# Kernel optimization log

Hardware: AMD Instinct MI355X
Metric: run time of the kernel (lower is better)

The kernel has to match this reference:

```python
import jax, jax.numpy as jnp
import numpy as np

EPS = 1e-9
CAPACITY_FACTOR = 1.25
MIN_EXPERT_CAPACITY = 4
SECOND_THRESHOLD = 0.2
LOSS_COEF = 0.01

B, N, D, E, H = 4, 2048, 1024, 16, 4096


def setup_inputs() -> dict:
    key = jax.random.key(0)
    k_x, k_g, k_w1, k_w2, k_n = jax.random.split(key, 5)
    return {
        "x": jax.random.normal(k_x, (B, N, D), dtype=jnp.float32),
        "w_gating": jax.random.normal(k_g, (D, E), dtype=jnp.float32) * 0.02,
        "w1": jax.random.normal(k_w1, (E, D, H), dtype=jnp.float32) * 0.02,
        "w2": jax.random.normal(k_w2, (E, H, D), dtype=jnp.float32) * 0.02,
        "noise": jax.random.uniform(k_n, (B, N), dtype=jnp.float32),
    }


def top2_gating(x, w_gating, noise):
    b, n, d = x.shape
    e = w_gating.shape[1]
    # static expert capacity (training-mode capacity factor)
    capacity = max(min(n, int((n * CAPACITY_FACTOR) / e)), MIN_EXPERT_CAPACITY)
    raw_gates = jax.nn.softmax(jnp.einsum('bnd,de->bne', x, w_gating), axis=-1)  # [b,n,e]

    index_1 = jnp.argmax(raw_gates, axis=-1)                     # [b,n]
    mask_1 = jax.nn.one_hot(index_1, e, dtype=raw_gates.dtype)   # [b,n,e]
    gate_1 = jnp.max(raw_gates, axis=-1)                         # [b,n]

    gates_wo1 = raw_gates * (1.0 - mask_1)
    index_2 = jnp.argmax(gates_wo1, axis=-1)
    mask_2 = jax.nn.one_hot(index_2, e, dtype=raw_gates.dtype)
    gate_2 = jnp.max(gates_wo1, axis=-1)

    denom = gate_1 + gate_2 + EPS
    gate_1 = gate_1 / denom
    gate_2 = gate_2 / denom

    # second policy == 'random': keep second expert with prob gate_2 / threshold
    keep_2 = (noise < gate_2 / max(SECOND_THRESHOLD, EPS)).astype(raw_gates.dtype)
    mask_2 = mask_2 * keep_2[..., None]

    # load-balancing auxiliary loss
    density_1 = jnp.mean(mask_1, axis=-2)          # [b,e]
    density_proxy = jnp.mean(raw_gates, axis=-2)   # [b,e]
    loss = jnp.mean(density_proxy * density_1) * float(e * e)

    # position of each token within its primary expert (exclusive cumsum)
    pos_1 = (jnp.cumsum(mask_1, axis=-2) - mask_1) * mask_1
    mask_1 = mask_1 * (pos_1 < capacity).astype(raw_gates.dtype)
    mask_1_count = jnp.sum(mask_1, axis=-2, keepdims=True)
    mask_1_flat = jnp.sum(mask_1, axis=-1)
    pos_1 = jnp.sum(pos_1, axis=-1).astype(jnp.int32)  # [b,n]
    gate_1 = gate_1 * mask_1_flat

    pos_2 = (jnp.cumsum(mask_2, axis=-2) - mask_2 + mask_1_count) * mask_2
    mask_2 = mask_2 * (pos_2 < capacity).astype(raw_gates.dtype)
    mask_2_flat = jnp.sum(mask_2, axis=-1)
    pos_2 = jnp.sum(pos_2, axis=-1).astype(jnp.int32)
    gate_2 = gate_2 * mask_2_flat

    # one_hot of out-of-range positions yields zeros == safe_one_hot[..., :capacity]
    combine = (
        gate_1[..., None, None] * mask_1_flat[..., None, None]
        * jax.nn.one_hot(index_1, e, dtype=raw_gates.dtype)[..., None]
        * jax.nn.one_hot(pos_1, capacity, dtype=raw_gates.dtype)[..., None, :]
        + gate_2[..., None, None] * mask_2_flat[..., None, None]
        * jax.nn.one_hot(index_2, e, dtype=raw_gates.dtype)[..., None]
        * jax.nn.one_hot(pos_2, capacity, dtype=raw_gates.dtype)[..., None, :]
    )  # [b,n,e,c]
    dispatch = (combine != 0).astype(combine.dtype)
    return dispatch, combine, loss


def reference(x, w_gating, w1, w2, noise):
    dispatch, combine, loss = top2_gating(x, w_gating, noise)
    expert_inputs = jnp.einsum('bnd,bnec->ebcd', x, dispatch)  # [e,b,c,d]
    e, b, c, d = expert_inputs.shape
    ei = expert_inputs.reshape(e, b * c, d)
    hidden = jax.nn.relu(jnp.einsum('etd,edh->eth', ei, w1))
    eo = jnp.einsum('eth,ehd->etd', hidden, w2).reshape(e, b, c, d)
    output = jnp.einsum('ebcd,bnec->bnd', eo, combine)
    return output, loss * LOSS_COEF
```

## Files before the change

### kernel.cpp

```cpp
#include <hip/hip_runtime.h>

#define BB 4
#define NT_TOK 2048
#define DD 1024
#define EE 16
#define HH 4096
#define CAP 160
#define NTOK (BB * NT_TOK)
#define MROWS (BB * CAP)

typedef __attribute__((ext_vector_type(4))) float floatx4;
typedef __attribute__((ext_vector_type(8))) short short8;

__device__ __forceinline__ ushort f2bf(float f) {
  union { float f; unsigned u; } v; v.f = f;
  unsigned u = v.u;
  return (ushort)((u + 0x7FFFu + ((u >> 16) & 1u)) >> 16);
}

__device__ __forceinline__ uint cvt_pk_bf16(float lo, float hi) {
  uint r;
  asm("v_cvt_pk_bf16_f32 %0, %1, %2" : "=v"(r) : "v"(lo), "v"(hi));
  return r;
}

__global__ __launch_bounds__(256)
void k_gating(const float* __restrict__ x, const float* __restrict__ wg,
              const float* __restrict__ noise,
              int* __restrict__ idx1, int* __restrict__ idx2,
              float* __restrict__ g1, float* __restrict__ g2,
              int* __restrict__ pos1, int* __restrict__ pos2,
              float* __restrict__ dp, float* __restrict__ d1)
{
  __shared__ float s_dp[EE];
  __shared__ float s_d1[EE];
  const int tid = threadIdx.x, lane = tid & 63, wave = tid >> 6;
  if (tid < EE) { s_dp[tid] = 0.f; s_d1[tid] = 0.f; }
  __syncthreads();

  const int t = blockIdx.x * 4 + wave;
  const int b = t / NT_TOK;

  float acc[EE];
#pragma unroll
  for (int e = 0; e < EE; ++e) acc[e] = 0.f;

  const float* xr = x + (size_t)t * DD;
#pragma unroll 4
  for (int i = 0; i < DD / 64; ++i) {
    const int d = i * 64 + lane;
    const float xv = xr[d];
    const float4* wr = (const float4*)(wg + (size_t)d * EE);
#pragma unroll
    for (int q = 0; q < 4; ++q) {
      const float4 w4 = wr[q];
      acc[q * 4 + 0] += xv * w4.x;
      acc[q * 4 + 1] += xv * w4.y;
      acc[q * 4 + 2] += xv * w4.z;
      acc[q * 4 + 3] += xv * w4.w;
    }
  }
#pragma unroll
  for (int off = 32; off >= 1; off >>= 1)
#pragma unroll
    for (int e = 0; e < EE; ++e) acc[e] += __shfl_xor(acc[e], off);

  float mx = acc[0];
#pragma unroll
  for (int e = 1; e < EE; ++e) mx = fmaxf(mx, acc[e]);
  float g[EE], s = 0.f;
#pragma unroll
  for (int e = 0; e < EE; ++e) { g[e] = expf(acc[e] - mx); s += g[e]; }
  const float inv = 1.f / s;
#pragma unroll
  for (int e = 0; e < EE; ++e) g[e] *= inv;

  int i1 = 0; float v1 = g[0];
#pragma unroll
  for (int e = 1; e < EE; ++e) if (g[e] > v1) { v1 = g[e]; i1 = e; }
  int i2 = -1; float v2 = -1.f;
#pragma unroll
  for (int e = 0; e < EE; ++e) if (e != i1 && g[e] > v2) { v2 = g[e]; i2 = e; }

  const float denom = v1 + v2 + 1e-9f;
  const float g1n = v1 / denom, g2n = v2 / denom;
  const bool keep2 = noise[t] < (g2n / 0.2f);

  if (lane == 0) {
    idx1[t] = i1;
    idx2[t] = keep2 ? i2 : -1;
    g1[t] = g1n; g2[t] = g2n;
    pos1[t] = -1; pos2[t] = -1;
  }
  if (lane < EE) atomicAdd(&s_dp[lane], g[lane]);
  if (lane == 0) atomicAdd(&s_d1[i1], 1.f);
  __syncthreads();
  if (tid < EE) {
    atomicAdd(&dp[b * EE + tid], s_dp[tid]);
    atomicAdd(&d1[b * EE + tid], s_d1[tid]);
  }
}

__global__ __launch_bounds__(64)
void k_scan(const int* __restrict__ idx1, const int* __restrict__ idx2,
            int* __restrict__ pos1, int* __restrict__ pos2,
            int* __restrict__ slot_tok)
{
  const int b = (int)blockIdx.x >> 4;
  const int e = (int)blockIdx.x & 15;
  const int lane = threadIdx.x;
  const unsigned long long lm = (1ull << lane) - 1ull;
  int* st = slot_tok + ((size_t)e * BB + b) * CAP;

  int v[NT_TOK / 64];
#pragma unroll
  for (int c = 0; c < NT_TOK / 64; ++c) v[c] = idx1[b * NT_TOK + c * 64 + lane];
  int base = 0;
  for (int c = 0; c < NT_TOK / 64; ++c) {
    const bool m = (v[c] == e);
    const unsigned long long bal = __ballot(m);
    if (m) {
      const int p = base + __popcll(bal & lm);
      if (p < CAP) { const int n = c * 64 + lane; pos1[b * NT_TOK + n] = p; st[p] = n; }
    }
    base += __popcll(bal);
  }
  const int count1 = base < CAP ? base : CAP;

#pragma unroll
  for (int c = 0; c < NT_TOK / 64; ++c) v[c] = idx2[b * NT_TOK + c * 64 + lane];
  base = count1;
  for (int c = 0; c < NT_TOK / 64; ++c) {
    const bool m = (v[c] == e);
    const unsigned long long bal = __ballot(m);
    if (m) {
      const int p = base + __popcll(bal & lm);
      if (p < CAP) { const int n = c * 64 + lane; pos2[b * NT_TOK + n] = p; st[p] = n; }
    }
    base += __popcll(bal);
  }
  const int used = base < CAP ? base : CAP;
  for (int p = used + lane; p < CAP; p += 64) st[p] = -1;
}

__global__ __launch_bounds__(256)
void k_gather(const float* __restrict__ x, const int* __restrict__ slot_tok,
              ushort* __restrict__ ei)
{
  const int s = blockIdx.x;
  const int tid = threadIdx.x;
  const int r = s % MROWS;
  const int b = r / CAP;
  const int tok = slot_tok[s];
  ushort4 o;
  if (tok >= 0) {
    const float4 v = *(const float4*)(x + ((size_t)b * NT_TOK + tok) * DD + tid * 4);
    o.x = f2bf(v.x); o.y = f2bf(v.y); o.z = f2bf(v.z); o.w = f2bf(v.w);
  } else {
    o.x = 0; o.y = 0; o.z = 0; o.w = 0;
  }
  *(ushort4*)(ei + (size_t)s * DD + tid * 4) = o;
}

template<int K, int NC, bool RELU_BF16>
__global__ __launch_bounds__(256)
void expert_gemm(const ushort* __restrict__ A, const float* __restrict__ W,
                 ushort* __restrict__ Cb, float* __restrict__ Cf)
{
  constexpr int MT = MROWS / 128;
  constexpr int NTl = NC / 128;
  constexpr int nwg = EE * MT * NTl;
  constexpr int NKT = K / 32;
  int wg = ((int)blockIdx.x & 7) * (nwg / 8) + ((int)blockIdx.x >> 3);
  const int mt = wg % MT; wg /= MT;
  const int nt = wg % NTl;
  const int e  = wg / NTl;
  const int m0 = mt * 128, n0 = nt * 128;

  __shared__ ushort As[2][128 * 32];
  __shared__ ushort Bs[2][128 * 32];

  const int tid = threadIdx.x;
  const int lane = tid & 63;
  const int wr = (tid >> 6) >> 1;
  const int wc = (tid >> 6) & 1;
  const int fr = lane & 15, fq = lane >> 4;

  const ushort* Ae = A + (size_t)e * MROWS * K;
  const float*  We = W + (size_t)e * K * NC;

  const int arow = tid >> 1;
  const int acol = (tid & 1) * 16;
  const int bn4 = (tid & 31) * 4;
  const int bk4 = (tid >> 5) * 4;

  const int ac0 = (tid & 1) * 2;
  const int aswz0 = arow * 32 + ((ac0       ^ ((arow >> 1) & 3)) << 3);
  const int aswz1 = arow * 32 + (((ac0 + 1) ^ ((arow >> 1) & 3)) << 3);
  const int bchunk = (tid >> 6);
  const int bh = ((tid >> 5) & 1) * 4;
  const int cswr = (fq ^ ((fr >> 1) & 3)) << 3;

  const ushort* Arow = Ae + (size_t)(m0 + arow) * K + acol;
  const float*  Wcol = We + n0 + bn4;

  floatx4 acc[4][4];
#pragma unroll
  for (int m = 0; m < 4; ++m)
#pragma unroll
    for (int n = 0; n < 4; ++n) acc[m][n] = (floatx4){0.f, 0.f, 0.f, 0.f};

  uint4 ra0, ra1;
  float wq[4][4];

  auto issue_loads = [&](int kt) {
    const uint4* ga = (const uint4*)(Arow + kt * 32);
    ra0 = ga[0];
    ra1 = ga[1];
#pragma unroll
    for (int kk = 0; kk < 4; ++kk) {
      const float4 f = *(const float4*)(Wcol + (size_t)(kt * 32 + bk4 + kk) * NC);
      wq[kk][0] = f.x; wq[kk][1] = f.y; wq[kk][2] = f.z; wq[kk][3] = f.w;
    }
  };
  auto write_lds = [&](int buf) {
    ushort* as_ = As[buf];
    ushort* bs_ = Bs[buf];
    *(uint4*)&as_[aswz0] = ra0;
    *(uint4*)&as_[aswz1] = ra1;
#pragma unroll
    for (int nn = 0; nn < 4; ++nn) {
      const int row = bn4 + nn;
      uint2 p;
      p.x = cvt_pk_bf16(wq[0][nn], wq[1][nn]);
      p.y = cvt_pk_bf16(wq[2][nn], wq[3][nn]);
      *(uint2*)&bs_[row * 32 + ((bchunk ^ ((row >> 1) & 3)) << 3) + bh] = p;
    }
  };

  issue_loads(0);
  write_lds(0);
  __syncthreads();

  for (int kt = 0; kt < NKT; ++kt) {
    const int cur = kt & 1;
    const bool more = (kt + 1 < NKT);
    if (more) issue_loads(kt + 1);

    const ushort* as_ = As[cur];
    const ushort* bs_ = Bs[cur];
    short8 af[4], bfr[4];
#pragma unroll
    for (int m = 0; m < 4; ++m)
      af[m] = *(const short8*)&as_[(wr * 64 + m * 16 + fr) * 32 + cswr];
#pragma unroll
    for (int n = 0; n < 4; ++n)
      bfr[n] = *(const short8*)&bs_[(wc * 64 + n * 16 + fr) * 32 + cswr];
#pragma unroll
    for (int m = 0; m < 4; ++m)
#pragma unroll
      for (int n = 0; n < 4; ++n)
        acc[m][n] = __builtin_amdgcn_mfma_f32_16x16x32_bf16(af[m], bfr[n], acc[m][n], 0, 0, 0);

    if (more) {
      write_lds(cur ^ 1);
      __syncthreads();
    }
  }

#pragma unroll
  for (int m = 0; m < 4; ++m) {
    const int row0 = m0 + wr * 64 + m * 16 + fq * 4;
#pragma unroll
    for (int n = 0; n < 4; ++n) {
      const int col = n0 + wc * 64 + n * 16 + fr;
#pragma unroll
      for (int j = 0; j < 4; ++j) {
        const size_t ci = ((size_t)e * MROWS + row0 + j) * NC + col;
        if constexpr (RELU_BF16) Cb[ci] = f2bf(fmaxf(acc[m][n][j], 0.f));
        else                     Cf[ci] = acc[m][n][j];
      }
    }
  }
}

__global__ __launch_bounds__(256)
void k_combine(const float* __restrict__ eo,
               const int* __restrict__ idx1, const int* __restrict__ idx2,
               const float* __restrict__ g1, const float* __restrict__ g2,
               const int* __restrict__ pos1, const int* __restrict__ pos2,
               float* __restrict__ out)
{
  const int t = blockIdx.x, tid = threadIdx.x;
  const int b = t / NT_TOK;
  float r0 = 0.f, r1 = 0.f, r2 = 0.f, r3 = 0.f;
  const int p1 = pos1[t];
  if (p1 >= 0) {
    const float g = g1[t];
    const float4 v = *(const float4*)(eo + ((size_t)idx1[t] * MROWS + b * CAP + p1) * DD + tid * 4);
    r0 += g * v.x; r1 += g * v.y; r2 += g * v.z; r3 += g * v.w;
  }
  const int p2 = pos2[t];
  if (p2 >= 0) {
    const float g = g2[t];
    const float4 v = *(const float4*)(eo + ((size_t)idx2[t] * MROWS + b * CAP + p2) * DD + tid * 4);
    r0 += g * v.x; r1 += g * v.y; r2 += g * v.z; r3 += g * v.w;
  }
  float4 o; o.x = r0; o.y = r1; o.z = r2; o.w = r3;
  *(float4*)(out + (size_t)t * DD + tid * 4) = o;
}

__global__ __launch_bounds__(64)
void k_loss(const float* __restrict__ dens, float* __restrict__ out_loss)
{
  const int lane = threadIdx.x;
  float v = (dens[lane] * (1.f / 2048.f)) * (dens[64 + lane] * (1.f / 2048.f));
#pragma unroll
  for (int off = 32; off >= 1; off >>= 1) v += __shfl_xor(v, off);
  if (lane == 0) out_loss[0] = (v / 64.f) * 256.f * 0.01f;
}

extern "C" void kernel_launch(void* const* d_in, const int* in_sizes, int n_in,
                              void* d_out, int out_size, void* d_ws, size_t ws_size,
                              hipStream_t stream)
{
  const float* x     = (const float*)d_in[0];
  const float* wgate = (const float*)d_in[1];
  const float* w1    = (const float*)d_in[2];
  const float* w2    = (const float*)d_in[3];
  const float* noise = (const float*)d_in[4];
  float* out = (float*)d_out;

  size_t off = 0;
  char* wsb = (char*)d_ws;
  auto alloc = [&](size_t bytes) -> void* {
    void* p = wsb + off;
    off += (bytes + 255) & ~(size_t)255;
    return p;
  };
  ushort* ei  = (ushort*)alloc((size_t)EE * MROWS * DD * 2);
  ushort* hid = (ushort*)alloc((size_t)EE * MROWS * HH * 2);
  float*  eo  = (float*) alloc((size_t)EE * MROWS * DD * 4);
  int*   idx1 = (int*)  alloc((size_t)NTOK * 4);
  int*   idx2 = (int*)  alloc((size_t)NTOK * 4);
  float* g1   = (float*)alloc((size_t)NTOK * 4);
  float* g2   = (float*)alloc((size_t)NTOK * 4);
  int*   pos1 = (int*)  alloc((size_t)NTOK * 4);
  int*   pos2 = (int*)  alloc((size_t)NTOK * 4);
  int* slot_tok = (int*)alloc((size_t)EE * BB * CAP * 4);
  float* dens = (float*)alloc(128 * 4);

  hipMemsetAsync(dens, 0, 128 * 4, stream);
  k_gating<<<NTOK / 4, 256, 0, stream>>>(x, wgate, noise, idx1, idx2, g1, g2,
                                         pos1, pos2, dens, dens + 64);
  k_scan<<<BB * EE, 64, 0, stream>>>(idx1, idx2, pos1, pos2, slot_tok);
  k_gather<<<EE * MROWS, 256, 0, stream>>>(x, slot_tok, ei);
  expert_gemm<DD, HH, true ><<<EE * (MROWS / 128) * (HH / 128), 256, 0, stream>>>(ei,  w1, hid, nullptr);
  expert_gemm<HH, DD, false><<<EE * (MROWS / 128) * (DD / 128), 256, 0, stream>>>(hid, w2, nullptr, eo);
  k_combine<<<NTOK, 256, 0, stream>>>(eo, idx1, idx2, g1, g2, pos1, pos2, out);
  k_loss<<<1, 64, 0, stream>>>(dens, out + (size_t)NTOK * DD);
}
```

Baseline: 447.0 us.

## Load A tiles directly into LDS and restructure B loads for vector LDS writes

The A operand (bf16 activations) now goes from global memory straight into LDS through global_load_lds, skipping the register staging and explicit LDS stores. The lane mapping applies the XOR swizzle on the global side so the LDS layout stays the same. The B (fp32 weights) loads are remapped so each thread reads 8 consecutive k values for a single n column, packs them to bf16 and writes one 16-byte LDS store per chunk instead of four 8-byte stores. The cost is scalar, strided 4-byte global loads for B (coalesced across lanes along n) and a dependence on correct completion ordering of the async LDS loads before the barrier.

```diff
diff --git a/kernel.cpp b/kernel.cpp
--- a/kernel.cpp
+++ b/kernel.cpp
@@ -22,6 +22,12 @@
   uint r;
   asm("v_cvt_pk_bf16_f32 %0, %1, %2" : "=v"(r) : "v"(lo), "v"(hi));
   return r;
+}
+
+__device__ __forceinline__ void gload_lds16(const void* g, void* l) {
+  __builtin_amdgcn_global_load_lds(
+      (const __attribute__((address_space(1))) unsigned*)g,
+      (__attribute__((address_space(3))) unsigned*)l, 16, 0, 0);
 }
 
 __global__ __launch_bounds__(256)
@@ -182,70 +188,65 @@
 
   const int tid = threadIdx.x;
   const int lane = tid & 63;
-  const int wr = (tid >> 6) >> 1;
-  const int wc = (tid >> 6) & 1;
+  const int wv = tid >> 6;
+  const int wr = wv >> 1;
+  const int wc = wv & 1;
   const int fr = lane & 15, fq = lane >> 4;
 
   const ushort* Ae = A + (size_t)e * MROWS * K;
   const float*  We = W + (size_t)e * K * NC;
 
-  const int arow = tid >> 1;
-  const int acol = (tid & 1) * 16;
-  const int bn4 = (tid & 31) * 4;
-  const int bk4 = (tid >> 5) * 4;
-
-  const int ac0 = (tid & 1) * 2;
-  const int aswz0 = arow * 32 + ((ac0       ^ ((arow >> 1) & 3)) << 3);
-  const int aswz1 = arow * 32 + (((ac0 + 1) ^ ((arow >> 1) & 3)) << 3);
-  const int bchunk = (tid >> 6);
-  const int bh = ((tid >> 5) & 1) * 4;
+  const int arow = wv * 32 + (lane >> 2);
+  const int lchunk = (lane & 3) ^ ((arow >> 1) & 3);
+  const ushort* Ag0 = Ae + (size_t)(m0 + arow) * K + lchunk * 8;
+  const ushort* Ag1 = Ag0 + (size_t)16 * K;
+  const int n_loc = tid & 127;
+  const int kc = tid >> 7;
+  const float* Wb = We + n0 + n_loc;
+  const int bswz0 = n_loc * 32 + (((kc)     ^ ((n_loc >> 1) & 3)) << 3);
+  const int bswz1 = n_loc * 32 + (((kc + 2) ^ ((n_loc >> 1) & 3)) << 3);
   const int cswr = (fq ^ ((fr >> 1) & 3)) << 3;
 
-  const ushort* Arow = Ae + (size_t)(m0 + arow) * K + acol;
-  const float*  Wcol = We + n0 + bn4;
-
   floatx4 acc[4][4];
 #pragma unroll
   for (int m = 0; m < 4; ++m)
 #pragma unroll
     for (int n = 0; n < 4; ++n) acc[m][n] = (floatx4){0.f, 0.f, 0.f, 0.f};
 
-  uint4 ra0, ra1;
-  float wq[4][4];
-
-  auto issue_loads = [&](int kt) {
-    const uint4* ga = (const uint4*)(Arow + kt * 32);
-    ra0 = ga[0];
-    ra1 = ga[1];
-#pragma unroll
-    for (int kk = 0; kk < 4; ++kk) {
-      const float4 f = *(const float4*)(Wcol + (size_t)(kt * 32 + bk4 + kk) * NC);
-      wq[kk][0] = f.x; wq[kk][1] = f.y; wq[kk][2] = f.z; wq[kk][3] = f.w;
-    }
+  float bq0[8], bq1[8];
+
+  auto issue_A = [&](int kt, int buf) {
+    gload_lds16(Ag0 + kt * 32, (void*)&As[buf][(wv * 32) * 32]);
+    gload_lds16(Ag1 + kt * 32, (void*)&As[buf][(wv * 32 + 16) * 32]);
   };
-  auto write_lds = [&](int buf) {
-    ushort* as_ = As[buf];
+  auto load_B = [&](int kt) {
+    const float* p0 = Wb + (size_t)(kt * 32 + kc * 8) * NC;
+    const float* p1 = Wb + (size_t)(kt * 32 + (kc + 2) * 8) * NC;
+#pragma unroll
+    for (int j = 0; j < 8; ++j) bq0[j] = p0[(size_t)j * NC];
+#pragma unroll
+    for (int j = 0; j < 8; ++j) bq1[j] = p1[(size_t)j * NC];
+  };
+  auto write_B = [&](int buf) {
     ushort* bs_ = Bs[buf];
-    *(uint4*)&as_[aswz0] = ra0;
-    *(uint4*)&as_[aswz1] = ra1;
-#pragma unroll
-    for (int nn = 0; nn < 4; ++nn) {
-      const int row = bn4 + nn;
-      uint2 p;
-      p.x = cvt_pk_bf16(wq[0][nn], wq[1][nn]);
-      p.y = cvt_pk_bf16(wq[2][nn], wq[3][nn]);
-      *(uint2*)&bs_[row * 32 + ((bchunk ^ ((row >> 1) & 3)) << 3) + bh] = p;
-    }
+    uint4 q;
+    q.x = cvt_pk_bf16(bq0[0], bq0[1]); q.y = cvt_pk_bf16(bq0[2], bq0[3]);
+    q.z = cvt_pk_bf16(bq0[4], bq0[5]); q.w = cvt_pk_bf16(bq0[6], bq0[7]);
+    *(uint4*)&bs_[bswz0] = q;
+    q.x = cvt_pk_bf16(bq1[0], bq1[1]); q.y = cvt_pk_bf16(bq1[2], bq1[3]);
+    q.z = cvt_pk_bf16(bq1[4], bq1[5]); q.w = cvt_pk_bf16(bq1[6], bq1[7]);
+    *(uint4*)&bs_[bswz1] = q;
   };
 
-  issue_loads(0);
-  write_lds(0);
+  issue_A(0, 0);
+  load_B(0);
+  write_B(0);
   __syncthreads();
 
   for (int kt = 0; kt < NKT; ++kt) {
     const int cur = kt & 1;
     const bool more = (kt + 1 < NKT);
-    if (more) issue_loads(kt + 1);
+    if (more) { issue_A(kt + 1, cur ^ 1); load_B(kt + 1); }
 
     const ushort* as_ = As[cur];
     const ushort* bs_ = Bs[cur];
@@ -263,7 +264,7 @@
         acc[m][n] = __builtin_amdgcn_mfma_f32_16x16x32_bf16(af[m], bfr[n], acc[m][n], 0, 0, 0);
 
     if (more) {
-      write_lds(cur ^ 1);
+      write_B(cur ^ 1);
       __syncthreads();
     }
   }
```

Result: slower. 464.4 us (+3.9%).
